# Kernel tuning notes

Measured on AMD Instinct MI355X. Metric: run time of the kernel, lower is better.

Reference implementation:

```python
import jax, jax.numpy as jnp
import numpy as np
import math

B, HQ, HK, M, N, D, S, O, SO = 4, 32, 8, 16, 8192, 128, 256, 8, 64


def _make_proj_score(key):
    # __init__: randn proj, then per-D-column-chunk QR (rot=True), scaled by sqrt(D)
    proj = jax.random.normal(key, (D, S), dtype=jnp.float32)
    chunks = []
    for i in range(0, S, D):
        q, _ = jnp.linalg.qr(proj[:, i:i + D])
        chunks.append(q)
    return (jnp.concatenate(chunks, axis=-1) * math.sqrt(D)).astype(jnp.float32)


def setup_inputs() -> dict:
    key = jax.random.key(0)
    k1, k2, k3, k4 = jax.random.split(key, 4)
    return {
        "query": jax.random.normal(k1, (B, HQ, M, D), dtype=jnp.float32),
        "data": jax.random.normal(k2, (B, HK, N, D), dtype=jnp.float32),
        "proj_dir_score": _make_proj_score(k3),
        "outlier_indices": jax.random.randint(k4, (B, HK, N, O), 0, D, dtype=jnp.int32),
        "dim_outlier": SO,
    }


def reference(query, data, proj_dir_score, outlier_indices, dim_outlier):
    # query: [B,Hq,M,D] fp32; data (keys): [B,Hk,N,D]; proj_dir_score: [D,S]
    Bb, Hk, Nn, Dd = data.shape
    Hq, Mq = query.shape[1], query.shape[2]
    G = Hq // Hk  # GQA repeat factor (repeat_interleave along heads)
    Ss = proj_dir_score.shape[1]
    So = dim_outlier
    dt = data.dtype

    # --- qjl_quant: split keys into inlier / outlier channels per key ---
    # scatter a 0/1 outlier-channel mask: [B,Hk,N,D]
    flat_idx = outlier_indices.reshape(-1, outlier_indices.shape[-1])
    rows = jnp.arange(flat_idx.shape[0])[:, None]
    mask = jnp.zeros((flat_idx.shape[0], Dd), dt).at[rows, flat_idx].set(1.0)
    mask = mask.reshape(Bb, Hk, Nn, Dd)

    k_out = data * mask          # outlier channels only
    k_in = data - k_out          # outlier channels zeroed
    norm_in = jnp.linalg.norm(k_in, axis=-1)    # [B,Hk,N]
    norm_out = jnp.linalg.norm(k_out, axis=-1)  # [B,Hk,N]

    # 1-bit sign-JL quantization (bit-packed in the CUDA kernel; +-1 floats here)
    sign_in = jnp.sign(jnp.einsum('bhnd,ds->bhns', k_in, proj_dir_score))   # [B,Hk,N,S]
    proj_out = proj_dir_score[:, :So]                                       # [D,So]
    sign_out = jnp.sign(jnp.einsum('bhnd,ds->bhns', k_out, proj_out))       # [B,Hk,N,So]

    # --- qjl_gqa_score: QJL unbiased inner-product estimator ---
    # <q,k> ~= sqrt(pi/2)/m * ||k|| * <S q, sign(S k)>, inlier + outlier parts
    coef_in = math.sqrt(math.pi / 2.0) / Ss
    coef_out = math.sqrt(math.pi / 2.0) / So

    k_eff = sign_in * (coef_in * norm_in)[..., None]                        # [B,Hk,N,S]
    # fold outlier part back onto head-dim channels: w_eff[n,d] = mask * (sign_out @ proj_out^T)
    w_eff = mask * jnp.einsum('bhns,ds->bhnd', sign_out, proj_out)
    w_eff = w_eff * (coef_out * norm_out)[..., None]                        # [B,Hk,N,D]

    sketched_q = jnp.einsum('bhmd,ds->bhms', query, proj_dir_score)         # [B,Hq,M,S]
    # group query heads per kv head instead of repeat_interleaving keys (same math)
    sq_g = sketched_q.reshape(Bb, Hk, G, Mq, Ss)
    q_g = query.reshape(Bb, Hk, G, Mq, Dd)

    scores = (jnp.einsum('bhgms,bhns->bhgmn', sq_g, k_eff)
              + jnp.einsum('bhgmd,bhnd->bhgmn', q_g, w_eff))                # [B,Hk,G,M,N]
    scores = scores.reshape(Bb, Hq, Mq, Nn)
    return jnp.swapaxes(scores, -1, -2)  # final .transpose(-1,-2): [B,Hq,N,M]
```

## Files before the change

kernel.cpp:

```cpp
#include <hip/hip_runtime.h>
#include <hip/hip_bf16.h>
#include <math.h>

namespace {
constexpr int B_ = 4, HQ_ = 32, HK_ = 8, G_ = 4, M_ = 16;
constexpr int N_ = 8192, D_ = 128, S_ = 256, O_ = 8;
constexpr int TN = 64;
constexpr float TAU = 4e-3f;
}

typedef short short8 __attribute__((ext_vector_type(8)));
typedef float f32x4 __attribute__((ext_vector_type(4)));
typedef unsigned int uint4_ __attribute__((ext_vector_type(4)));

__device__ inline unsigned short f2bf_rne(float f) {
    unsigned u = __float_as_uint(f);
    u += 0x7FFF + ((u >> 16) & 1);
    return (unsigned short)(u >> 16);
}
__device__ inline float bf2f(unsigned short h) {
    return __uint_as_float(((unsigned)h) << 16);
}

__global__ __launch_bounds__(256) void qjl_prept(const float* __restrict__ P,
                                                 unsigned short* __restrict__ PtHi,
                                                 unsigned short* __restrict__ PtLo,
                                                 float* __restrict__ Pt32) {
    const int d = blockIdx.x;
    const int s = threadIdx.x;
    const float f = P[d * S_ + s];
    const unsigned short hb = f2bf_rne(f);
    const float lof = f - bf2f(hb);
    PtHi[s * D_ + d] = hb;
    PtLo[s * D_ + d] = f2bf_rne(lof);
    Pt32[s * D_ + d] = f;
}

__global__ __launch_bounds__(256) void qjl_sketch_q(const float* __restrict__ q,
                                                    const float* __restrict__ P,
                                                    unsigned short* __restrict__ sqHi) {
    __shared__ float qs[M_][D_];
    const int tid = threadIdx.x;
    const size_t blk = blockIdx.x;
    const float* qb = q + blk * (size_t)(M_ * D_);
    for (int i = tid; i < M_ * D_ / 4; i += 256)
        reinterpret_cast<float4*>(&qs[0][0])[i] = reinterpret_cast<const float4*>(qb)[i];
    __syncthreads();
    float acc[M_];
#pragma unroll
    for (int m = 0; m < M_; ++m) acc[m] = 0.f;
    const int s = tid;
    for (int d = 0; d < D_; ++d) {
        const float pv = P[d * S_ + s];
#pragma unroll
        for (int m = 0; m < M_; ++m) acc[m] = fmaf(qs[m][d], pv, acc[m]);
    }
    unsigned short* ob = sqHi + blk * (size_t)(M_ * S_);
#pragma unroll
    for (int m = 0; m < M_; ++m) ob[m * S_ + s] = f2bf_rne(acc[m]);
}

__device__ __noinline__ float qjl_fix_coop(const float* __restrict__ drow,
                                           const float* __restrict__ Pt32,
                                           int col, unsigned long long ip,
                                           float a, int src) {
    const int lane = threadIdx.x & 63;
    const float2 dv = *reinterpret_cast<const float2*>(&drow[2 * lane]);
    const float2 pv = *reinterpret_cast<const float2*>(&Pt32[(size_t)col * D_ + 2 * lane]);
    double p = 0.0;
#pragma unroll
    for (int e = 0; e < 2; ++e) {
        const int d = 2 * lane + e;
        const float v = e ? dv.y : dv.x;
        const float pw = e ? pv.y : pv.x;
        bool isout = false;
#pragma unroll
        for (int j = 0; j < 8; ++j)
            isout = isout || (((unsigned)(ip >> (8 * j)) & 0xFFu) == (unsigned)d);
        if (!isout) p = fma((double)v, (double)pw, p);
    }
#pragma unroll
    for (int off = 1; off < 64; off <<= 1) p += __shfl_xor(p, off);
    if (lane == src) a = (p > 0.0) ? 1.f : -1.f;
    return a;
}

__global__ __launch_bounds__(256) void qjl_main(const float* __restrict__ data,
                                                const float* __restrict__ q,
                                                const float* __restrict__ P,
                                                const int* __restrict__ oidx,
                                                const unsigned short* __restrict__ sqHi,
                                                const unsigned short* __restrict__ PtHi,
                                                const unsigned short* __restrict__ PtLo,
                                                const float* __restrict__ Pt32,
                                                float* __restrict__ out) {
    __shared__ unsigned short abuf[16384];
    __shared__ unsigned long long words[4][16][4];
    __shared__ float su2[TN][O_];
    __shared__ unsigned long long sidxp[TN];
    __shared__ float sfull[TN];
    __shared__ float snin[TN];
    __shared__ float snout[TN];

    const int tid = threadIdx.x;
    const int lane = tid & 63;
    const int wv = tid >> 6;
    const int l15 = lane & 15;
    const int kgrp = (lane >> 4) << 3;
    const int nt = blockIdx.x, hk = blockIdx.y, b = blockIdx.z;
    const int n0 = nt * TN;
    const float* dbase = data + ((size_t)(b * HK_ + hk) * N_) * D_;

    {
        const int r = tid >> 2;
        const int c = tid & 3;
        const float* drow = dbase + (size_t)(n0 + r) * D_;
        const int swz = (r & 7) << 3;
        float ssq = 0.f;
#pragma unroll
        for (int k = 0; k < 8; ++k) {
            const int f = c + 4 * k;
            float4 v = reinterpret_cast<const float4*>(drow)[f];
            ssq += v.x * v.x + v.y * v.y + v.z * v.z + v.w * v.w;
            unsigned short h0 = f2bf_rne(v.x), h1 = f2bf_rne(v.y),
                           h2 = f2bf_rne(v.z), h3 = f2bf_rne(v.w);
            unsigned short l0 = f2bf_rne(v.x - bf2f(h0)), l1 = f2bf_rne(v.y - bf2f(h1)),
                           l2 = f2bf_rne(v.z - bf2f(h2)), l3 = f2bf_rne(v.w - bf2f(h3));
            const int ei = r * 128 + ((4 * f) ^ swz);
            unsigned long long hw = (unsigned long long)h0 | ((unsigned long long)h1 << 16) |
                                    ((unsigned long long)h2 << 32) | ((unsigned long long)h3 << 48);
            unsigned long long lw = (unsigned long long)l0 | ((unsigned long long)l1 << 16) |
                                    ((unsigned long long)l2 << 32) | ((unsigned long long)l3 << 48);
            *reinterpret_cast<unsigned long long*>(&abuf[ei]) = hw;
            *reinterpret_cast<unsigned long long*>(&abuf[8192 + ei]) = lw;
        }
        ssq += __shfl_xor(ssq, 1);
        ssq += __shfl_xor(ssq, 2);
        if (c == 0) sfull[r] = ssq;
    }
    __syncthreads();

    if (tid < TN) {
        const int n = tid;
        const int* ob = oidx + ((size_t)(b * HK_ + hk) * N_ + n0 + n) * O_;
        const float* drow = dbase + (size_t)(n0 + n) * D_;
        int id[O_];
        int4 i0 = reinterpret_cast<const int4*>(ob)[0];
        int4 i1 = reinterpret_cast<const int4*>(ob)[1];
        id[0] = i0.x; id[1] = i0.y; id[2] = i0.z; id[3] = i0.w;
        id[4] = i1.x; id[5] = i1.y; id[6] = i1.z; id[7] = i1.w;
        const int swz = (n & 7) << 3;
        unsigned long long ip = 0;
        float so2 = 0.f;
#pragma unroll
        for (int j = 0; j < O_; ++j) {
            bool dup = false;
#pragma unroll
            for (int jj = 0; jj < O_; ++jj)
                if (jj < j) dup = dup || (id[jj] == id[j]);
            if (!dup) {
                const float v = drow[id[j]];
                so2 = fmaf(v, v, so2);
                ip |= (unsigned long long)(id[j] & 0xFF) << (8 * j);
                const int ei = n * 128 + (id[j] ^ swz);
                abuf[ei] = 0;
                abuf[8192 + ei] = 0;
            } else {
                ip |= 0xFFull << (8 * j);
            }
        }
        sidxp[n] = ip;
        const float CIN = (float)(1.2533141373155003 / 256.0);
        const float COUT = (float)(1.2533141373155003 / 64.0);
        snin[n] = CIN * sqrtf(fmaxf(sfull[n] - so2, 0.f));
        snout[n] = COUT * sqrtf(so2);
    }
    __syncthreads();

    {
        const int n = tid >> 2;
        const int c = tid & 3;
        const unsigned long long ip = sidxp[n];
        const float* drow = dbase + (size_t)(n0 + n) * D_;
        float u[O_], vv[O_];
        const float* pr[O_];
        bool val[O_];
#pragma unroll
        for (int j = 0; j < O_; ++j) {
            u[j] = 0.f;
            const unsigned bt = (unsigned)(ip >> (8 * j)) & 0xFFu;
            val[j] = (bt != 0xFFu);
            const int ix = (int)(bt & 0x7Fu);
            pr[j] = P + ix * S_;
            vv[j] = val[j] ? drow[ix] : 0.f;
        }
#pragma unroll
        for (int ch = 0; ch < 4; ++ch) {
            const int tc = c * 16 + ch * 4;
            float4 pj[O_];
#pragma unroll
            for (int j = 0; j < O_; ++j)
                pj[j] = *reinterpret_cast<const float4*>(pr[j] + tc);
#pragma unroll
            for (int e = 0; e < 4; ++e) {
                double cs = 0.0;
#pragma unroll
                for (int j = 0; j < O_; ++j)
                    cs = fma((double)vv[j], (double)pj[j][e], cs);
                const float sg = (cs > 0.0) ? 1.f : ((cs < 0.0) ? -1.f : 0.f);
#pragma unroll
                for (int j = 0; j < O_; ++j)
                    u[j] = fmaf(sg, pj[j][e], u[j]);
            }
        }
#pragma unroll
        for (int j = 0; j < O_; ++j) {
            u[j] += __shfl_xor(u[j], 1);
            u[j] += __shfl_xor(u[j], 2);
        }
        if (c == 0) {
            const float cno = snout[n];
#pragma unroll
            for (int j = 0; j < O_; ++j) su2[n][j] = val[j] ? u[j] * cno : 0.f;
        }
    }

    short8 bhi[2][4], blo[2][4];
    const int t0 = wv * 4;
#define QJL_LOADB(buf, ti)                                                         \
    do {                                                                           \
        const size_t bo = (size_t)(16 * (t0 + (ti)) + l15) * D_ + kgrp;            \
        _Pragma("unroll") for (int ks = 0; ks < 4; ++ks) {                         \
            bhi[buf][ks] = *reinterpret_cast<const short8*>(PtHi + bo + ks * 32);  \
            blo[buf][ks] = *reinterpret_cast<const short8*>(PtLo + bo + ks * 32);  \
        }                                                                          \
    } while (0)
    QJL_LOADB(0, 0);
    __syncthreads();

    {
#pragma unroll
        for (int ti = 0; ti < 4; ++ti) {
            if (ti < 3) {
                if ((ti & 1) == 0) QJL_LOADB(1, ti + 1);
                else               QJL_LOADB(0, ti + 1);
            }
            const int cur = ti & 1;
            const int t = t0 + ti;
#pragma unroll
            for (int rt = 0; rt < 4; ++rt) {
                const int arow = 16 * rt + l15;
                const int aswz = (arow & 7) << 3;
                short8 ahi[4], alo[4];
#pragma unroll
                for (int ks = 0; ks < 4; ++ks) {
                    const int ei = arow * 128 + ((ks * 32 + kgrp) ^ aswz);
                    ahi[ks] = *reinterpret_cast<const short8*>(&abuf[ei]);
                    alo[ks] = *reinterpret_cast<const short8*>(&abuf[8192 + ei]);
                }
                f32x4 acc = (f32x4){0.f, 0.f, 0.f, 0.f};
#pragma unroll
                for (int ks = 0; ks < 4; ++ks) {
                    acc = __builtin_amdgcn_mfma_f32_16x16x32_bf16(ahi[ks], bhi[cur][ks], acc, 0, 0, 0);
                    acc = __builtin_amdgcn_mfma_f32_16x16x32_bf16(ahi[ks], blo[cur][ks], acc, 0, 0, 0);
                    acc = __builtin_amdgcn_mfma_f32_16x16x32_bf16(alo[ks], bhi[cur][ks], acc, 0, 0, 0);
                }
#pragma unroll
                for (int r = 0; r < 4; ++r) {
                    float a = acc[r];
                    unsigned long long low = __ballot(fabsf(a) < TAU);
                    while (low) {
                        const int src = __ffsll((unsigned long long)low) - 1;
                        low &= low - 1;
                        const int row = 16 * rt + ((src >> 4) << 2) + r;
                        const int col = 16 * t + (src & 15);
                        a = qjl_fix_coop(dbase + (size_t)(n0 + row) * D_, Pt32, col,
                                         sidxp[row], a, src);
                    }
                    const unsigned long long bb = __ballot(a > 0.f);
                    if (lane == 0) words[rt][t][r] = bb;
                }
            }
        }
    }
#undef QJL_LOADB

    const int hq = hk * G_ + wv;
    const unsigned short* sqb = sqHi + (size_t)(b * HQ_ + hq) * (M_ * S_);
    short8 aq[8];
#pragma unroll
    for (int ks = 0; ks < 8; ++ks)
        aq[ks] = *reinterpret_cast<const short8*>(sqb + (size_t)l15 * S_ + ks * 32 + kgrp);
    __syncthreads();

    {
        const int n = tid & 63;
        const int c64 = tid >> 6;
        const unsigned short cb = f2bf_rne(snin[n]);
        const unsigned base = (unsigned)cb | ((unsigned)cb << 16);
        const int g = (n >> 2) & 3;
        const int r = n & 3;
        const int w = n >> 4;
        const int swz = (n & 7) << 3;
#pragma unroll
        for (int i = 0; i < 4; ++i) {
            const int t = c64 * 4 + i;
            const unsigned long long wd = words[w][t][r];
            const unsigned bits = (unsigned)(wd >> (16 * g)) & 0xFFFFu;
            const unsigned nb = ~bits;
            unsigned o[8];
#pragma unroll
            for (int p = 0; p < 8; ++p) {
                const unsigned m = (((nb >> (2 * p)) & 1u) << 15) |
                                   (((nb >> (2 * p + 1)) & 1u) << 31);
                o[p] = base ^ m;
            }
            const int s0 = c64 * 64 + i * 16;
            const int e0 = n * 256 + (s0 ^ swz);
            const int e1 = n * 256 + ((s0 + 8) ^ swz);
            *reinterpret_cast<uint4_*>(&abuf[e0]) = (uint4_){o[0], o[1], o[2], o[3]};
            *reinterpret_cast<uint4_*>(&abuf[e1]) = (uint4_){o[4], o[5], o[6], o[7]};
        }
    }
    __syncthreads();

    {
        const float* qhead = q + (size_t)(b * HQ_ + hq) * (M_ * D_);
        const int m0 = (lane >> 4) << 2;
#pragma unroll
        for (int ct = 0; ct < 4; ++ct) {
            const int n = 16 * ct + l15;
            const f32x4 s01 = *reinterpret_cast<const f32x4*>(&su2[n][0]);
            const f32x4 s23 = *reinterpret_cast<const f32x4*>(&su2[n][4]);
            const unsigned long long ip = sidxp[n];
            float a0 = 0.f, a1 = 0.f, a2 = 0.f, a3 = 0.f;
#pragma unroll
            for (int j = 0; j < O_; ++j) {
                const float uj = (j < 4) ? s01[j & 3] : s23[j & 3];
                const int ix = (int)((ip >> (8 * j)) & 0x7Fu);
                const float* qp = qhead + ix;
                a0 = fmaf(uj, qp[(m0 + 0) * D_], a0);
                a1 = fmaf(uj, qp[(m0 + 1) * D_], a1);
                a2 = fmaf(uj, qp[(m0 + 2) * D_], a2);
                a3 = fmaf(uj, qp[(m0 + 3) * D_], a3);
            }
            f32x4 acc = (f32x4){a0, a1, a2, a3};
            const int nswz = (n & 7) << 3;
#pragma unroll
            for (int ks = 0; ks < 8; ++ks) {
                const int ei = n * 256 + ((ks * 32 + kgrp) ^ nswz);
                const short8 bs = *reinterpret_cast<const short8*>(&abuf[ei]);
                acc = __builtin_amdgcn_mfma_f32_16x16x32_bf16(aq[ks], bs, acc, 0, 0, 0);
            }
            float* ob = out + ((size_t)(b * HQ_ + hq) * N_ + (n0 + n)) * M_ + m0;
            *reinterpret_cast<f32x4*>(ob) = acc;
        }
    }
}

extern "C" void kernel_launch(void* const* d_in, const int* in_sizes, int n_in,
                              void* d_out, int out_size, void* d_ws, size_t ws_size,
                              hipStream_t stream) {
    const float* query = (const float*)d_in[0];
    const float* data  = (const float*)d_in[1];
    const float* proj  = (const float*)d_in[2];
    const int*   oidx  = (const int*)d_in[3];

    float* out = (float*)d_out;
    unsigned short* sqHi = (unsigned short*)d_ws;
    unsigned short* PtHi = (unsigned short*)((char*)d_ws + (1 << 20));
    unsigned short* PtLo = (unsigned short*)((char*)d_ws + (1 << 20) + (64 << 10));
    float*          Pt32 = (float*)((char*)d_ws + (1 << 20) + (128 << 10));

    qjl_prept<<<dim3(D_), dim3(S_), 0, stream>>>(proj, PtHi, PtLo, Pt32);
    qjl_sketch_q<<<dim3(B_ * HQ_), dim3(256), 0, stream>>>(query, proj, sqHi);
    qjl_main<<<dim3(N_ / TN, HK_, B_), dim3(256), 0, stream>>>(data, query, proj, oidx,
                                                               sqHi, PtHi, PtLo, Pt32, out);
}
```

Before: 254.5 us.

## Split MFMA accumulators, add wave-level fix-up early exit, lower TAU threshold

Lowers the sign-fix threshold TAU so fewer near-zero projections go through the cooperative fp32 recompute. The three chained bf16 MFMAs now feed three independent accumulators, which shortens the dependency chain, and a single wave ballot skips the per-row fix-up loop when no value is near zero. The double-buffered B-fragment prefetch is dropped in favour of plain per-tile loads, and the score MFMA is moved ahead of the outlier gather. A lower TAU risks more sign errors from bf16 rounding, and removing the prefetch may expose global load latency.

```diff
diff --git a/kernel.cpp b/kernel.cpp
--- a/kernel.cpp
+++ b/kernel.cpp
@@ -6,7 +6,7 @@
 constexpr int B_ = 4, HQ_ = 32, HK_ = 8, G_ = 4, M_ = 16;
 constexpr int N_ = 8192, D_ = 128, S_ = 256, O_ = 8;
 constexpr int TN = 64;
-constexpr float TAU = 4e-3f;
+constexpr float TAU = 1e-3f;
 }
 
 typedef short short8 __attribute__((ext_vector_type(8)));
@@ -225,28 +225,18 @@
         }
     }
 
-    short8 bhi[2][4], blo[2][4];
-    const int t0 = wv * 4;
-#define QJL_LOADB(buf, ti)                                                         \
-    do {                                                                           \
-        const size_t bo = (size_t)(16 * (t0 + (ti)) + l15) * D_ + kgrp;            \
-        _Pragma("unroll") for (int ks = 0; ks < 4; ++ks) {                         \
-            bhi[buf][ks] = *reinterpret_cast<const short8*>(PtHi + bo + ks * 32);  \
-            blo[buf][ks] = *reinterpret_cast<const short8*>(PtLo + bo + ks * 32);  \
-        }                                                                          \
-    } while (0)
-    QJL_LOADB(0, 0);
-    __syncthreads();
-
-    {
+    {
+        const int t0 = wv * 4;
 #pragma unroll
         for (int ti = 0; ti < 4; ++ti) {
-            if (ti < 3) {
-                if ((ti & 1) == 0) QJL_LOADB(1, ti + 1);
-                else               QJL_LOADB(0, ti + 1);
-            }
-            const int cur = ti & 1;
             const int t = t0 + ti;
+            short8 bhi[4], blo[4];
+            const size_t bo = (size_t)(16 * t + l15) * D_ + kgrp;
+#pragma unroll
+            for (int ks = 0; ks < 4; ++ks) {
+                bhi[ks] = *reinterpret_cast<const short8*>(PtHi + bo + ks * 32);
+                blo[ks] = *reinterpret_cast<const short8*>(PtLo + bo + ks * 32);
+            }
 #pragma unroll
             for (int rt = 0; rt < 4; ++rt) {
                 const int arow = 16 * rt + l15;
@@ -258,32 +248,40 @@
                     ahi[ks] = *reinterpret_cast<const short8*>(&abuf[ei]);
                     alo[ks] = *reinterpret_cast<const short8*>(&abuf[8192 + ei]);
                 }
-                f32x4 acc = (f32x4){0.f, 0.f, 0.f, 0.f};
+                f32x4 ac1 = (f32x4){0.f, 0.f, 0.f, 0.f};
+                f32x4 ac2 = (f32x4){0.f, 0.f, 0.f, 0.f};
+                f32x4 ac3 = (f32x4){0.f, 0.f, 0.f, 0.f};
 #pragma unroll
                 for (int ks = 0; ks < 4; ++ks) {
-                    acc = __builtin_amdgcn_mfma_f32_16x16x32_bf16(ahi[ks], bhi[cur][ks], acc, 0, 0, 0);
-                    acc = __builtin_amdgcn_mfma_f32_16x16x32_bf16(ahi[ks], blo[cur][ks], acc, 0, 0, 0);
-                    acc = __builtin_amdgcn_mfma_f32_16x16x32_bf16(alo[ks], bhi[cur][ks], acc, 0, 0, 0);
+                    ac1 = __builtin_amdgcn_mfma_f32_16x16x32_bf16(ahi[ks], bhi[ks], ac1, 0, 0, 0);
+                    ac2 = __builtin_amdgcn_mfma_f32_16x16x32_bf16(ahi[ks], blo[ks], ac2, 0, 0, 0);
+                    ac3 = __builtin_amdgcn_mfma_f32_16x16x32_bf16(alo[ks], bhi[ks], ac3, 0, 0, 0);
                 }
+                f32x4 a = (ac1 + ac2) + ac3;
+                const float mn = fminf(fminf(fabsf(a[0]), fabsf(a[1])),
+                                       fminf(fabsf(a[2]), fabsf(a[3])));
+                if (__ballot(mn < TAU) != 0ull) {
+#pragma unroll
+                    for (int r = 0; r < 4; ++r) {
+                        unsigned long long low = __ballot(fabsf(a[r]) < TAU);
+                        while (low) {
+                            const int src = __ffsll((unsigned long long)low) - 1;
+                            low &= low - 1;
+                            const int row = 16 * rt + ((src >> 4) << 2) + r;
+                            const int col = 16 * t + (src & 15);
+                            a[r] = qjl_fix_coop(dbase + (size_t)(n0 + row) * D_, Pt32, col,
+                                                sidxp[row], a[r], src);
+                        }
+                    }
+                }
 #pragma unroll
                 for (int r = 0; r < 4; ++r) {
-                    float a = acc[r];
-                    unsigned long long low = __ballot(fabsf(a) < TAU);
-                    while (low) {
-                        const int src = __ffsll((unsigned long long)low) - 1;
-                        low &= low - 1;
-                        const int row = 16 * rt + ((src >> 4) << 2) + r;
-                        const int col = 16 * t + (src & 15);
-                        a = qjl_fix_coop(dbase + (size_t)(n0 + row) * D_, Pt32, col,
-                                         sidxp[row], a, src);
-                    }
-                    const unsigned long long bb = __ballot(a > 0.f);
+                    const unsigned long long bb = __ballot(a[r] > 0.f);
                     if (lane == 0) words[rt][t][r] = bb;
                 }
             }
         }
     }
-#undef QJL_LOADB
 
     const int hq = hk * G_ + wv;
     const unsigned short* sqb = sqHi + (size_t)(b * HQ_ + hq) * (M_ * S_);
@@ -330,6 +328,14 @@
 #pragma unroll
         for (int ct = 0; ct < 4; ++ct) {
             const int n = 16 * ct + l15;
+            const int nswz = (n & 7) << 3;
+            f32x4 acc = (f32x4){0.f, 0.f, 0.f, 0.f};
+#pragma unroll
+            for (int ks = 0; ks < 8; ++ks) {
+                const int ei = n * 256 + ((ks * 32 + kgrp) ^ nswz);
+                const short8 bs = *reinterpret_cast<const short8*>(&abuf[ei]);
+                acc = __builtin_amdgcn_mfma_f32_16x16x32_bf16(aq[ks], bs, acc, 0, 0, 0);
+            }
             const f32x4 s01 = *reinterpret_cast<const f32x4*>(&su2[n][0]);
             const f32x4 s23 = *reinterpret_cast<const f32x4*>(&su2[n][4]);
             const unsigned long long ip = sidxp[n];
@@ -344,14 +350,7 @@
                 a2 = fmaf(uj, qp[(m0 + 2) * D_], a2);
                 a3 = fmaf(uj, qp[(m0 + 3) * D_], a3);
             }
-            f32x4 acc = (f32x4){a0, a1, a2, a3};
-            const int nswz = (n & 7) << 3;
-#pragma unroll
-            for (int ks = 0; ks < 8; ++ks) {
-                const int ei = n * 256 + ((ks * 32 + kgrp) ^ nswz);
-                const short8 bs = *reinterpret_cast<const short8*>(&abuf[ei]);
-                acc = __builtin_amdgcn_mfma_f32_16x16x32_bf16(aq[ks], bs, acc, 0, 0, 0);
-            }
+            acc[0] += a0; acc[1] += a1; acc[2] += a2; acc[3] += a3;
             float* ob = out + ((size_t)(b * HQ_ + hq) * N_ + (n0 + n)) * M_ + m0;
             *reinterpret_cast<f32x4*>(ob) = acc;
         }
```

Measured after the change: 250.9 us. About the same (-1.4%).
